# Optimization experiments

Measured on AMD Instinct MI355X. Metric: run time of the kernel, lower is better.

The kernel has to match this reference:

```python
import jax, jax.numpy as jnp
import numpy as np

N_NODES = 50000
N_EDGES = 800000
IN_DIM = 96
HID = 96


def setup_inputs() -> dict:
    key = jax.random.key(0)
    k1, k2, k3, k4 = jax.random.split(key, 4)
    x = jax.random.normal(k1, (N_NODES, IN_DIM), dtype=jnp.float32)
    edge_index = jax.random.randint(k2, (2, N_EDGES), 0, N_NODES, dtype=jnp.int64)
    s1 = 1.0 / np.sqrt(IN_DIM)
    s2 = 1.0 / np.sqrt(HID)
    W1 = jax.random.normal(k3, (IN_DIM, HID), dtype=jnp.float32) * s1
    b1 = jnp.zeros((HID,), dtype=jnp.float32)
    W2 = jax.random.normal(k4, (HID, HID), dtype=jnp.float32) * s2
    b2 = jnp.zeros((HID,), dtype=jnp.float32)
    return {"x": x, "edge_index": edge_index, "W1": W1, "b1": b1, "W2": W2, "b2": b2}


def _gcn_conv(x, src, dst, norm, W, b, n_nodes):
    # x' = D^{-1/2}(A+I)D^{-1/2} X W + b  (PyG GCNConv semantics)
    xw = x @ W                           # [N, out]
    msg = xw[src] * norm[:, None]        # gather + edge-normalize, [E+N, out]
    agg = jax.ops.segment_sum(msg, dst, num_segments=n_nodes)  # scatter-add
    return agg + b


def reference(x, edge_index, W1, b1, W2, b2):
    n_nodes = x.shape[0]
    loops = jnp.arange(n_nodes, dtype=edge_index.dtype)
    src = jnp.concatenate([edge_index[0], loops])  # sources (j)
    dst = jnp.concatenate([edge_index[1], loops])  # targets (i), aggregation index
    # symmetric normalization with self-loops; degree counted at targets
    deg = jax.ops.segment_sum(jnp.ones(dst.shape, dtype=x.dtype), dst, num_segments=n_nodes)
    dinv = jnp.where(deg > 0, jax.lax.rsqrt(deg), 0.0)
    norm = dinv[src] * dinv[dst]
    h = jax.nn.relu(_gcn_conv(x, src, dst, norm, W1, b1, n_nodes))
    h = jax.nn.relu(_gcn_conv(h, src, dst, norm, W2, b2, n_nodes))
    return h
```

## Files before the change

### kernel.cpp

```cpp
#include <hip/hip_runtime.h>

#define N_NODES 50000
#define N_EDGES 800000
#define DIM 96
#define FEAT_ELEMS (N_NODES * DIM)
#define NBLK 196

typedef __attribute__((ext_vector_type(8))) short short8;
typedef __attribute__((ext_vector_type(4))) float float4v;

__device__ __forceinline__ float bf16_to_f32(unsigned short u) {
    unsigned int w = ((unsigned int)u) << 16;
    float f;
    __builtin_memcpy(&f, &w, 4);
    return f;
}
__device__ __forceinline__ unsigned short f32_to_bf16_rne(float f) {
    unsigned int w;
    __builtin_memcpy(&w, &f, 4);
    unsigned int r = (w + 0x7FFFu + ((w >> 16) & 1u)) >> 16;
    return (unsigned short)r;
}

__device__ __forceinline__ int edge_at(const void* ep, int is64, int idx) {
    if (is64) return (int)((const long long*)ep)[idx];
    return ((const int*)ep)[idx];
}

__global__ __launch_bounds__(256) void prolog_kernel(const unsigned int* edges,
                                                     const unsigned int* x,
                                                     int* flagE, int* flagF, int* cnt) {
    __shared__ unsigned int sh[256];
    int t = threadIdx.x;
    int b = blockIdx.x;
    if (b < NBLK) {
        int i = b * 256 + t;
        if (i < N_NODES) cnt[i] = 0;
        return;
    }
    if (b == NBLK) {
        if (t < 64) {
            unsigned int acc = 0;
            for (int k = 0; k < 4; ++k) {
                int idx = t * 4 + k;
                int pos = 1 + 2 * idx * 3109;
                acc |= edges[pos];
            }
            sh[t] = acc;
        }
        __syncthreads();
        if (t == 0) {
            unsigned int a = 0;
            for (int i = 0; i < 64; ++i) a |= sh[i];
            *flagE = (a == 0u) ? 1 : 0;
        }
        return;
    }
    unsigned int w = x[t * 9000];
    unsigned int e = (w >> 7) & 0xFFu;
    sh[t] = (e >= 100u && e <= 135u) ? 1u : 0u;
    __syncthreads();
    if (t == 0) {
        int c = 0;
        for (int i = 0; i < 256; ++i) c += (int)sh[i];
        *flagF = (c >= 128) ? 1 : 0;
    }
}

__global__ __launch_bounds__(256) void count_compact_kernel(const void* edges,
                                                            const int* flagE, int* cnt,
                                                            unsigned short* srcu,
                                                            unsigned short* dstu,
                                                            unsigned short* rank) {
    int e = blockIdx.x * 256 + threadIdx.x;
    if (e >= N_EDGES) return;
    int is64 = *flagE;
    int s = edge_at(edges, is64, e);
    int d = edge_at(edges, is64, N_EDGES + e);
    srcu[e] = (unsigned short)s;
    dstu[e] = (unsigned short)d;
    rank[e] = (unsigned short)atomicAdd(&cnt[d], 1);
}

__global__ __launch_bounds__(256) void scan_blocksum_kernel(const int* cnt, int* blockSums) {
    __shared__ int sh[256];
    int i = blockIdx.x * 256 + threadIdx.x;
    sh[threadIdx.x] = (i < N_NODES) ? cnt[i] : 0;
    __syncthreads();
    for (int off = 128; off > 0; off >>= 1) {
        if (threadIdx.x < off) sh[threadIdx.x] += sh[threadIdx.x + off];
        __syncthreads();
    }
    if (threadIdx.x == 0) blockSums[blockIdx.x] = sh[0];
}

__global__ __launch_bounds__(256) void scan_offsets_kernel(const int* blockSums,
                                                           int* blockOffs, int* row_ptr) {
    __shared__ int sh[256];
    int t = threadIdx.x;
    int v = (t < NBLK) ? blockSums[t] : 0;
    sh[t] = v;
    __syncthreads();
    for (int off = 1; off < 256; off <<= 1) {
        int u = (t >= off) ? sh[t - off] : 0;
        __syncthreads();
        sh[t] += u;
        __syncthreads();
    }
    if (t < NBLK) blockOffs[t] = sh[t] - v;
    if (t == 255) row_ptr[N_NODES] = sh[255];
}

__global__ __launch_bounds__(256) void scan_apply_kernel(const int* cnt, const int* blockOffs,
                                                         int* row_ptr, float* dinv) {
    __shared__ int sh[256];
    int t = threadIdx.x;
    int i = blockIdx.x * 256 + t;
    int c = (i < N_NODES) ? cnt[i] : 0;
    sh[t] = c;
    __syncthreads();
    for (int off = 1; off < 256; off <<= 1) {
        int u = (t >= off) ? sh[t - off] : 0;
        __syncthreads();
        sh[t] += u;
        __syncthreads();
    }
    if (i < N_NODES) {
        int excl = sh[t] - c + blockOffs[blockIdx.x];
        row_ptr[i] = excl;
        dinv[i]    = rsqrtf((float)(c + 1));
    }
}

__global__ __launch_bounds__(256) void fill_direct_kernel(const unsigned short* __restrict__ dstu,
                                                          const unsigned short* __restrict__ srcu,
                                                          const unsigned short* __restrict__ rank,
                                                          const int* __restrict__ row_ptr,
                                                          unsigned short* __restrict__ csr_src) {
    int e = blockIdx.x * 256 + threadIdx.x;
    if (e >= N_EDGES) return;
    int d = dstu[e];
    int pos = row_ptr[d] + (int)rank[e];
    csr_src[pos] = srcu[e];
}

__global__ __launch_bounds__(256) void convert_kernel(const void* x, const int* flagF,
                                                      unsigned short* xb) {
    int i4 = (blockIdx.x * 256 + threadIdx.x) * 4;
    if (i4 >= FEAT_ELEMS) return;
    int isbf16 = *flagF;
    ushort4 o;
    if (isbf16) {
        o = *(const ushort4*)((const unsigned short*)x + i4);
    } else {
        float4 v = *(const float4*)((const float*)x + i4);
        o.x = f32_to_bf16_rne(v.x);
        o.y = f32_to_bf16_rne(v.y);
        o.z = f32_to_bf16_rne(v.z);
        o.w = f32_to_bf16_rne(v.w);
    }
    *(ushort4*)(xb + i4) = o;
}

__global__ __launch_bounds__(256) void gather_kernel(const unsigned short* __restrict__ feat,
                                                     const int* __restrict__ row_ptr,
                                                     const unsigned short* __restrict__ csr_src,
                                                     const float* __restrict__ dinv,
                                                     unsigned short* __restrict__ aggb) {
    int gid = blockIdx.x * 256 + threadIdx.x;
    int g = gid >> 4;
    int lane = gid & 15;
    if (g >= N_NODES) return;
    float di = dinv[g];
    int gb = g * DIM + lane * 2;
    ushort2 sv0 = *(const ushort2*)&feat[gb];
    ushort2 sv1 = *(const ushort2*)&feat[gb + 32];
    ushort2 sv2 = *(const ushort2*)&feat[gb + 64];
    float wself = di * di;
    float a0 = wself * bf16_to_f32(sv0.x), a1 = wself * bf16_to_f32(sv0.y);
    float a2 = wself * bf16_to_f32(sv1.x), a3 = wself * bf16_to_f32(sv1.y);
    float a4 = wself * bf16_to_f32(sv2.x), a5 = wself * bf16_to_f32(sv2.y);
    int e = row_ptr[g], e1 = row_ptr[g + 1];
    for (; e + 2 <= e1; e += 2) {
        int s0 = csr_src[e];
        int s1 = csr_src[e + 1];
        float w0 = dinv[s0] * di;
        float w1 = dinv[s1] * di;
        int b0 = s0 * DIM + lane * 2;
        int b1 = s1 * DIM + lane * 2;
        ushort2 p0 = *(const ushort2*)&feat[b0];
        ushort2 p1 = *(const ushort2*)&feat[b0 + 32];
        ushort2 p2 = *(const ushort2*)&feat[b0 + 64];
        ushort2 q0 = *(const ushort2*)&feat[b1];
        ushort2 q1 = *(const ushort2*)&feat[b1 + 32];
        ushort2 q2 = *(const ushort2*)&feat[b1 + 64];
        a0 = fmaf(w0, bf16_to_f32(p0.x), a0);  a1 = fmaf(w0, bf16_to_f32(p0.y), a1);
        a2 = fmaf(w0, bf16_to_f32(p1.x), a2);  a3 = fmaf(w0, bf16_to_f32(p1.y), a3);
        a4 = fmaf(w0, bf16_to_f32(p2.x), a4);  a5 = fmaf(w0, bf16_to_f32(p2.y), a5);
        a0 = fmaf(w1, bf16_to_f32(q0.x), a0);  a1 = fmaf(w1, bf16_to_f32(q0.y), a1);
        a2 = fmaf(w1, bf16_to_f32(q1.x), a2);  a3 = fmaf(w1, bf16_to_f32(q1.y), a3);
        a4 = fmaf(w1, bf16_to_f32(q2.x), a4);  a5 = fmaf(w1, bf16_to_f32(q2.y), a5);
    }
    if (e < e1) {
        int s = csr_src[e];
        float w = dinv[s] * di;
        int b0 = s * DIM + lane * 2;
        ushort2 p0 = *(const ushort2*)&feat[b0];
        ushort2 p1 = *(const ushort2*)&feat[b0 + 32];
        ushort2 p2 = *(const ushort2*)&feat[b0 + 64];
        a0 = fmaf(w, bf16_to_f32(p0.x), a0);  a1 = fmaf(w, bf16_to_f32(p0.y), a1);
        a2 = fmaf(w, bf16_to_f32(p1.x), a2);  a3 = fmaf(w, bf16_to_f32(p1.y), a3);
        a4 = fmaf(w, bf16_to_f32(p2.x), a4);  a5 = fmaf(w, bf16_to_f32(p2.y), a5);
    }
    unsigned int o0 = (unsigned int)f32_to_bf16_rne(a0) | ((unsigned int)f32_to_bf16_rne(a1) << 16);
    unsigned int o1 = (unsigned int)f32_to_bf16_rne(a2) | ((unsigned int)f32_to_bf16_rne(a3) << 16);
    unsigned int o2 = (unsigned int)f32_to_bf16_rne(a4) | ((unsigned int)f32_to_bf16_rne(a5) << 16);
    *(unsigned int*)&aggb[gb]      = o0;
    *(unsigned int*)&aggb[gb + 32] = o1;
    *(unsigned int*)&aggb[gb + 64] = o2;
}

__global__ __launch_bounds__(256) void gemm_mfma_kernel(const unsigned short* __restrict__ A,
                                                        const void* W, const void* bias,
                                                        const int* flagF,
                                                        void* out, int outMode) {
    __shared__ unsigned short Wlin[DIM * DIM];
    __shared__ unsigned short Wsw[3 * 6 * 64 * 8];
    __shared__ float bs[DIM];
    int wBf16 = *flagF;
    int outBf16 = (outMode == 2) ? wBf16 : outMode;

    if (wBf16) {
        const ushort4* W4 = (const ushort4*)W;
        ushort4* L4 = (ushort4*)Wlin;
        for (int i = threadIdx.x; i < DIM * DIM / 4; i += 256) L4[i] = W4[i];
        if (threadIdx.x < DIM)
            bs[threadIdx.x] = bf16_to_f32(((const unsigned short*)bias)[threadIdx.x]);
    } else {
        const float* Wf = (const float*)W;
        for (int i = threadIdx.x; i < DIM * DIM; i += 256) Wlin[i] = f32_to_bf16_rne(Wf[i]);
        if (threadIdx.x < DIM) bs[threadIdx.x] = ((const float*)bias)[threadIdx.x];
    }
    __syncthreads();

    for (int f = threadIdx.x; f < 1152; f += 256) {
        int kt = f / 384;
        int rem = f - kt * 384;
        int nt = rem >> 6;
        int ln64 = rem & 63;
        int q = ln64 >> 4, ln = ln64 & 15;
        int k0 = kt * 32 + q * 8;
        int n = nt * 16 + ln;
        unsigned int w0 = (unsigned int)Wlin[(k0 + 0) * DIM + n] |
                          ((unsigned int)Wlin[(k0 + 1) * DIM + n] << 16);
        unsigned int w1 = (unsigned int)Wlin[(k0 + 2) * DIM + n] |
                          ((unsigned int)Wlin[(k0 + 3) * DIM + n] << 16);
        unsigned int w2 = (unsigned int)Wlin[(k0 + 4) * DIM + n] |
                          ((unsigned int)Wlin[(k0 + 5) * DIM + n] << 16);
        unsigned int w3 = (unsigned int)Wlin[(k0 + 6) * DIM + n] |
                          ((unsigned int)Wlin[(k0 + 7) * DIM + n] << 16);
        uint4 pk = make_uint4(w0, w1, w2, w3);
        *(uint4*)&Wsw[f * 8] = pk;
    }
    __syncthreads();

    int wave = threadIdx.x >> 6;
    int lane = threadIdx.x & 63;
    int quad = lane >> 4, ln = lane & 15;
    int m0 = blockIdx.x * 64 + wave * 16;
    int arow = m0 + ln;
    bool arowok = (arow < N_NODES);

    float4v acc[6];
    #pragma unroll
    for (int nt = 0; nt < 6; ++nt) acc[nt] = (float4v){0.f, 0.f, 0.f, 0.f};

    #pragma unroll
    for (int kt = 0; kt < 3; ++kt) {
        short8 af;
        if (arowok) {
            af = *(const short8*)&A[arow * DIM + kt * 32 + quad * 8];
        } else {
            af = (short8){0, 0, 0, 0, 0, 0, 0, 0};
        }
        #pragma unroll
        for (int nt = 0; nt < 6; ++nt) {
            short8 bf = *(const short8*)&Wsw[((kt * 6 + nt) * 64 + lane) * 8];
            acc[nt] = __builtin_amdgcn_mfma_f32_16x16x32_bf16(af, bf, acc[nt], 0, 0, 0);
        }
    }

    #pragma unroll
    for (int nt = 0; nt < 6; ++nt) {
        int n = nt * 16 + ln;
        float bv = bs[n];
        #pragma unroll
        for (int reg = 0; reg < 4; ++reg) {
            int row = m0 + quad * 4 + reg;
            if (row >= N_NODES) continue;
            float v = fmaxf(acc[nt][reg] + bv, 0.0f);
            if (outBf16) ((unsigned short*)out)[row * DIM + n] = f32_to_bf16_rne(v);
            else         ((float*)out)[row * DIM + n] = v;
        }
    }
}

extern "C" void kernel_launch(void* const* d_in, const int* in_sizes, int n_in,
                              void* d_out, int out_size, void* d_ws, size_t ws_size,
                              hipStream_t stream) {
    const void* x  = d_in[0];
    const void* ei = d_in[1];
    const void* W1 = d_in[2];
    const void* b1 = d_in[3];
    const void* W2 = d_in[4];
    const void* b2 = d_in[5];

    char* base = (char*)d_ws;
    size_t off = 0;
    auto carve = [&](size_t bytes) -> void* {
        void* p = base + off;
        off += (bytes + 255) & ~(size_t)255;
        return p;
    };
    int*            flagE     = (int*)carve(4);
    int*            flagF     = (int*)carve(4);
    int*            cnt       = (int*)carve((size_t)N_NODES * 4);
    int*            row_ptr   = (int*)carve((size_t)(N_NODES + 1) * 4);
    float*          dinv      = (float*)carve((size_t)N_NODES * 4);
    int*            blockSums = (int*)carve((size_t)NBLK * 4);
    int*            blockOffs = (int*)carve((size_t)NBLK * 4);
    unsigned short* srcu      = (unsigned short*)carve((size_t)N_EDGES * 2);
    unsigned short* dstu      = (unsigned short*)carve((size_t)N_EDGES * 2);
    unsigned short* rank      = (unsigned short*)carve((size_t)N_EDGES * 2);
    unsigned short* csr_src   = (unsigned short*)carve((size_t)N_EDGES * 2);
    unsigned short* aggb      = (unsigned short*)carve((size_t)FEAT_ELEMS * 2);
    unsigned short* xb        = (unsigned short*)carve((size_t)FEAT_ELEMS * 2);
    unsigned short* h         = (unsigned short*)carve((size_t)FEAT_ELEMS * 2);

    const int egrid = (N_EDGES + 255) / 256;
    const int cgrid = (FEAT_ELEMS / 4 + 255) / 256;
    const int agrid = (N_NODES * 16 + 255) / 256;
    const int ggrid = (N_NODES + 63) / 64;

    prolog_kernel<<<NBLK + 2, 256, 0, stream>>>((const unsigned int*)ei,
                                                (const unsigned int*)x, flagE, flagF, cnt);
    count_compact_kernel<<<egrid, 256, 0, stream>>>(ei, flagE, cnt, srcu, dstu, rank);
    scan_blocksum_kernel<<<NBLK, 256, 0, stream>>>(cnt, blockSums);
    scan_offsets_kernel<<<1, 256, 0, stream>>>(blockSums, blockOffs, row_ptr);
    scan_apply_kernel<<<NBLK, 256, 0, stream>>>(cnt, blockOffs, row_ptr, dinv);
    fill_direct_kernel<<<egrid, 256, 0, stream>>>(dstu, srcu, rank, row_ptr, csr_src);
    convert_kernel<<<cgrid, 256, 0, stream>>>(x, flagF, xb);

    gather_kernel<<<agrid, 256, 0, stream>>>(xb, row_ptr, csr_src, dinv, aggb);
    gemm_mfma_kernel<<<ggrid, 256, 0, stream>>>(aggb, W1, b1, flagF, h, 1);

    gather_kernel<<<agrid, 256, 0, stream>>>(h, row_ptr, csr_src, dinv, aggb);
    gemm_mfma_kernel<<<ggrid, 256, 0, stream>>>(aggb, W2, b2, flagF, d_out, 2);
}
```

Before: 212.3 us.

## Partition CSR fill by XCD destination range and widen gather loads

Result: slower. 217.8 us (+2.6%).

```diff
diff --git a/kernel.cpp b/kernel.cpp
--- a/kernel.cpp
+++ b/kernel.cpp
@@ -5,6 +5,9 @@
 #define DIM 96
 #define FEAT_ELEMS (N_NODES * DIM)
 #define NBLK 196
+#define NODES_PER_XCD 6250
+#define FILL_CHUNK 2048
+#define FILL_GRID (391 * 8)
 
 typedef __attribute__((ext_vector_type(8))) short short8;
 typedef __attribute__((ext_vector_type(4))) float float4v;
@@ -132,16 +135,25 @@
     }
 }
 
-__global__ __launch_bounds__(256) void fill_direct_kernel(const unsigned short* __restrict__ dstu,
-                                                          const unsigned short* __restrict__ srcu,
-                                                          const unsigned short* __restrict__ rank,
-                                                          const int* __restrict__ row_ptr,
-                                                          unsigned short* __restrict__ csr_src) {
-    int e = blockIdx.x * 256 + threadIdx.x;
-    if (e >= N_EDGES) return;
-    int d = dstu[e];
-    int pos = row_ptr[d] + (int)rank[e];
-    csr_src[pos] = srcu[e];
+__global__ __launch_bounds__(256) void fill_xcd_kernel(const unsigned short* __restrict__ dstu,
+                                                       const unsigned short* __restrict__ srcu,
+                                                       const unsigned short* __restrict__ rank,
+                                                       const int* __restrict__ row_ptr,
+                                                       unsigned short* __restrict__ csr_src) {
+    int xcd = blockIdx.x & 7;
+    int chunk = blockIdx.x >> 3;
+    int d0 = xcd * NODES_PER_XCD;
+    int d1 = d0 + NODES_PER_XCD;
+    int e0 = chunk * FILL_CHUNK;
+    #pragma unroll
+    for (int i = 0; i < FILL_CHUNK / 256; ++i) {
+        int e = e0 + i * 256 + threadIdx.x;
+        if (e >= N_EDGES) break;
+        int d = dstu[e];
+        if (d >= d0 && d < d1) {
+            csr_src[row_ptr[d] + (int)rank[e]] = srcu[e];
+        }
+    }
 }
 
 __global__ __launch_bounds__(256) void convert_kernel(const void* x, const int* flagF,
@@ -172,52 +184,50 @@
     int lane = gid & 15;
     if (g >= N_NODES) return;
     float di = dinv[g];
-    int gb = g * DIM + lane * 2;
-    ushort2 sv0 = *(const ushort2*)&feat[gb];
-    ushort2 sv1 = *(const ushort2*)&feat[gb + 32];
-    ushort2 sv2 = *(const ushort2*)&feat[gb + 64];
+    int o4 = lane * 4;
+    int o2 = 64 + lane * 2;
+    int gbase = g * DIM;
+    ushort4 sv = *(const ushort4*)&feat[gbase + o4];
+    ushort2 sw = *(const ushort2*)&feat[gbase + o2];
     float wself = di * di;
-    float a0 = wself * bf16_to_f32(sv0.x), a1 = wself * bf16_to_f32(sv0.y);
-    float a2 = wself * bf16_to_f32(sv1.x), a3 = wself * bf16_to_f32(sv1.y);
-    float a4 = wself * bf16_to_f32(sv2.x), a5 = wself * bf16_to_f32(sv2.y);
+    float a0 = wself * bf16_to_f32(sv.x), a1 = wself * bf16_to_f32(sv.y);
+    float a2 = wself * bf16_to_f32(sv.z), a3 = wself * bf16_to_f32(sv.w);
+    float a4 = wself * bf16_to_f32(sw.x), a5 = wself * bf16_to_f32(sw.y);
     int e = row_ptr[g], e1 = row_ptr[g + 1];
     for (; e + 2 <= e1; e += 2) {
         int s0 = csr_src[e];
         int s1 = csr_src[e + 1];
         float w0 = dinv[s0] * di;
         float w1 = dinv[s1] * di;
-        int b0 = s0 * DIM + lane * 2;
-        int b1 = s1 * DIM + lane * 2;
-        ushort2 p0 = *(const ushort2*)&feat[b0];
-        ushort2 p1 = *(const ushort2*)&feat[b0 + 32];
-        ushort2 p2 = *(const ushort2*)&feat[b0 + 64];
-        ushort2 q0 = *(const ushort2*)&feat[b1];
-        ushort2 q1 = *(const ushort2*)&feat[b1 + 32];
-        ushort2 q2 = *(const ushort2*)&feat[b1 + 64];
-        a0 = fmaf(w0, bf16_to_f32(p0.x), a0);  a1 = fmaf(w0, bf16_to_f32(p0.y), a1);
-        a2 = fmaf(w0, bf16_to_f32(p1.x), a2);  a3 = fmaf(w0, bf16_to_f32(p1.y), a3);
-        a4 = fmaf(w0, bf16_to_f32(p2.x), a4);  a5 = fmaf(w0, bf16_to_f32(p2.y), a5);
-        a0 = fmaf(w1, bf16_to_f32(q0.x), a0);  a1 = fmaf(w1, bf16_to_f32(q0.y), a1);
-        a2 = fmaf(w1, bf16_to_f32(q1.x), a2);  a3 = fmaf(w1, bf16_to_f32(q1.y), a3);
-        a4 = fmaf(w1, bf16_to_f32(q2.x), a4);  a5 = fmaf(w1, bf16_to_f32(q2.y), a5);
+        int b0 = s0 * DIM;
+        int b1 = s1 * DIM;
+        ushort4 p = *(const ushort4*)&feat[b0 + o4];
+        ushort2 pw = *(const ushort2*)&feat[b0 + o2];
+        ushort4 q = *(const ushort4*)&feat[b1 + o4];
+        ushort2 qw = *(const ushort2*)&feat[b1 + o2];
+        a0 = fmaf(w0, bf16_to_f32(p.x), a0);  a1 = fmaf(w0, bf16_to_f32(p.y), a1);
+        a2 = fmaf(w0, bf16_to_f32(p.z), a2);  a3 = fmaf(w0, bf16_to_f32(p.w), a3);
+        a4 = fmaf(w0, bf16_to_f32(pw.x), a4); a5 = fmaf(w0, bf16_to_f32(pw.y), a5);
+        a0 = fmaf(w1, bf16_to_f32(q.x), a0);  a1 = fmaf(w1, bf16_to_f32(q.y), a1);
+        a2 = fmaf(w1, bf16_to_f32(q.z), a2);  a3 = fmaf(w1, bf16_to_f32(q.w), a3);
+        a4 = fmaf(w1, bf16_to_f32(qw.x), a4); a5 = fmaf(w1, bf16_to_f32(qw.y), a5);
     }
     if (e < e1) {
         int s = csr_src[e];
         float w = dinv[s] * di;
-        int b0 = s * DIM + lane * 2;
-        ushort2 p0 = *(const ushort2*)&feat[b0];
-        ushort2 p1 = *(const ushort2*)&feat[b0 + 32];
-        ushort2 p2 = *(const ushort2*)&feat[b0 + 64];
-        a0 = fmaf(w, bf16_to_f32(p0.x), a0);  a1 = fmaf(w, bf16_to_f32(p0.y), a1);
-        a2 = fmaf(w, bf16_to_f32(p1.x), a2);  a3 = fmaf(w, bf16_to_f32(p1.y), a3);
-        a4 = fmaf(w, bf16_to_f32(p2.x), a4);  a5 = fmaf(w, bf16_to_f32(p2.y), a5);
-    }
-    unsigned int o0 = (unsigned int)f32_to_bf16_rne(a0) | ((unsigned int)f32_to_bf16_rne(a1) << 16);
-    unsigned int o1 = (unsigned int)f32_to_bf16_rne(a2) | ((unsigned int)f32_to_bf16_rne(a3) << 16);
-    unsigned int o2 = (unsigned int)f32_to_bf16_rne(a4) | ((unsigned int)f32_to_bf16_rne(a5) << 16);
-    *(unsigned int*)&aggb[gb]      = o0;
-    *(unsigned int*)&aggb[gb + 32] = o1;
-    *(unsigned int*)&aggb[gb + 64] = o2;
+        int b0 = s * DIM;
+        ushort4 p = *(const ushort4*)&feat[b0 + o4];
+        ushort2 pw = *(const ushort2*)&feat[b0 + o2];
+        a0 = fmaf(w, bf16_to_f32(p.x), a0);  a1 = fmaf(w, bf16_to_f32(p.y), a1);
+        a2 = fmaf(w, bf16_to_f32(p.z), a2);  a3 = fmaf(w, bf16_to_f32(p.w), a3);
+        a4 = fmaf(w, bf16_to_f32(pw.x), a4); a5 = fmaf(w, bf16_to_f32(pw.y), a5);
+    }
+    uint2 ov;
+    ov.x = (unsigned int)f32_to_bf16_rne(a0) | ((unsigned int)f32_to_bf16_rne(a1) << 16);
+    ov.y = (unsigned int)f32_to_bf16_rne(a2) | ((unsigned int)f32_to_bf16_rne(a3) << 16);
+    unsigned int ow = (unsigned int)f32_to_bf16_rne(a4) | ((unsigned int)f32_to_bf16_rne(a5) << 16);
+    *(uint2*)&aggb[gbase + o4] = ov;
+    *(unsigned int*)&aggb[gbase + o2] = ow;
 }
 
 __global__ __launch_bounds__(256) void gemm_mfma_kernel(const unsigned short* __restrict__ A,
@@ -348,7 +358,7 @@
     scan_blocksum_kernel<<<NBLK, 256, 0, stream>>>(cnt, blockSums);
     scan_offsets_kernel<<<1, 256, 0, stream>>>(blockSums, blockOffs, row_ptr);
     scan_apply_kernel<<<NBLK, 256, 0, stream>>>(cnt, blockOffs, row_ptr, dinv);
-    fill_direct_kernel<<<egrid, 256, 0, stream>>>(dstu, srcu, rank, row_ptr, csr_src);
+    fill_xcd_kernel<<<FILL_GRID, 256, 0, stream>>>(dstu, srcu, rank, row_ptr, csr_src);
     convert_kernel<<<cgrid, 256, 0, stream>>>(x, flagF, xb);
 
     gather_kernel<<<agrid, 256, 0, stream>>>(xb, row_ptr, csr_src, dinv, aggb);
```
